# Optimization experiments

Measured on AMD Instinct MI355X. Metric: run time of the kernel, lower is better.

## Reference

```python
import jax, jax.numpy as jnp
import numpy as np

S, TM1, B, V, E, H = 96, 96, 8, 32000, 256, 512
PAD = 0
NEG = -1e30


def setup_inputs() -> dict:
    key = jax.random.key(0)
    ks = jax.random.split(key, 10)
    n = lambda k, shape, s=0.05: (jax.random.normal(k, shape, jnp.float32) * s)
    return {
        "src": jax.random.randint(ks[0], (S, B), 0, V, jnp.int32),
        "tgt": jax.random.randint(ks[1], (TM1 + 1, B), 0, V, jnp.int32),
        "emb": n(ks[2], (V, E)),
        "W_ih": n(ks[3], (4 * H, E)),
        "W_hh": n(ks[4], (4 * H, H)),
        "b_ih": jnp.zeros((4 * H,), jnp.float32),
        "b_hh": jnp.zeros((4 * H,), jnp.float32),
        "W_att": n(ks[5], (H, H)),
        "sent": n(ks[6], (H,)),
        "W_read": n(ks[7], (V, H)),
    }


def _lstm_cell(x, h, c, W_ih, W_hh, b_ih, b_hh):
    g = x @ W_ih.T + b_ih + h @ W_hh.T + b_hh
    i, f, gg, o = jnp.split(g, 4, axis=-1)
    c = jax.nn.sigmoid(f) * c + jax.nn.sigmoid(i) * jnp.tanh(gg)
    h = jax.nn.sigmoid(o) * jnp.tanh(c)
    return h, c


def _forward(src, tgt, emb, W_ih, W_hh, b_ih, b_hh, W_att, sent, W_read):
    # padding_idx behavior: pad row of embedding is zero (and gets no grad)
    emb_eff = emb * (jnp.arange(V) != PAD).astype(emb.dtype)[:, None]
    xs = jnp.concatenate([emb_eff[src], emb_eff[tgt[:-1]]], axis=0)  # [S+TM1,B,E]

    def step(carry, x):
        h, c = carry
        h, c = _lstm_cell(x, h, c, W_ih, W_hh, b_ih, b_hh)
        return (h, c), h

    init = (jnp.zeros((B, H), xs.dtype), jnp.zeros((B, H), xs.dtype))
    _, H_all = jax.lax.scan(step, init, xs)  # [S+TM1,B,H]

    H_dec = H_all[S:]                              # [TM1,B,H]
    Q = jnp.tanh(H_dec @ W_att.T)                  # [TM1,B,H]
    Z = jnp.einsum("tbh,jbh->tjb", Q, H_all)      # [TM1,S+TM1,B]
    zs = jnp.einsum("tbh,h->tb", Q, sent)         # sentinel logit
    logits = jnp.concatenate([Z, zs[:, None, :]], axis=1)  # [TM1,S+TM1+1,B]

    j = jnp.arange(S + TM1 + 1)
    t = jnp.arange(TM1)
    valid = (j[None, :] < S + t[:, None] + 1) | (j[None, :] == S + TM1)
    logits = jnp.where(valid[:, :, None], logits, NEG)
    a = jax.nn.softmax(logits, axis=1)
    a_src, a_tgt, a_sent = a[:, :S], a[:, S:S + TM1], a[:, -1]

    # pointer distributions via scatter-add (avoids dense one-hot [S,B,V])
    b_idx = jnp.arange(B)[None, None, :]
    t_idx = jnp.arange(TM1)[:, None, None]
    p_ptr = jnp.zeros((TM1, B, V), a.dtype)
    p_ptr = p_ptr.at[t_idx, b_idx, src[None, :, :]].add(a_src)
    p_ptr = p_ptr.at[t_idx, b_idx, tgt[:-1][None, :, :]].add(a_tgt)

    p_vocab = jax.nn.softmax(H_dec @ W_read.T, axis=-1)  # [TM1,B,V]
    p = p_ptr + p_vocab * a_sent[:, :, None]
    ptr_scores = p_ptr + a_sent[:, :, None]

    mask = (tgt != PAD).astype(p.dtype)  # [TM1+1,B]
    gold = jnp.take_along_axis(jnp.log(p), tgt[1:][:, :, None], axis=2)[..., 0] * mask[1:]
    gold_ptr = jnp.take_along_axis(jnp.log(ptr_scores), tgt[1:][:, :, None], axis=2)[..., 0] * mask[1:]
    return gold.sum(0), gold_ptr.sum(0)  # ([B], [B])


def reference(src, tgt, emb, W_ih, W_hh, b_ih, b_hh, W_att, sent, W_read):
    return _forward(src, tgt, emb, W_ih, W_hh, b_ih, b_hh, W_att, sent, W_read)
```

## Files before the change

### kernel.cpp

```cpp
#include <hip/hip_runtime.h>
#include <hip/hip_cooperative_groups.h>
#include <math.h>

#define SS   96
#define TM   96
#define BB   8
#define VV   32000
#define EE   256
#define HH   512
#define NTOK (SS + TM)
#define G4   (4 * HH)
#define NEGF (-1e30f)
#define NBLK 64

typedef __attribute__((ext_vector_type(8))) short short8;
typedef __attribute__((ext_vector_type(4))) float f32x4;

#define XIH_OFF   ((size_t)0)
#define XIH_SZ    ((size_t)NTOK * BB * G4)
#define HALL_OFF  (XIH_OFF + XIH_SZ)
#define HALL_SZ   ((size_t)NTOK * BB * HH)
#define Q_OFF     (HALL_OFF + HALL_SZ)
#define Q_SZ      ((size_t)TM * BB * HH)
#define PPTR_OFF  (Q_OFF + Q_SZ)
#define ASENT_OFF (PPTR_OFF + (size_t)(TM * BB))
#define SSUM_OFF  (ASENT_OFF + (size_t)(TM * BB))
#define LSTAR_OFF (SSUM_OFF + (size_t)(TM * BB))
#define BAR_OFF   (LSTAR_OFF + (size_t)(TM * BB))
#define ABF_OFF   (BAR_OFF + (size_t)1024)
#define ABF_SZF   ((size_t)(768 * HH) / 2)
#define WBF_OFF   (ABF_OFF + ABF_SZF)
#define WBF_SZF   ((size_t)VV * HH / 2)
#define NEED_F    (WBF_OFF + WBF_SZF)

__device__ __forceinline__ float sigf(float x) { return 1.f / (1.f + __expf(-x)); }

__global__ void __launch_bounds__(256) k_xih(const int* __restrict__ src,
                                             const int* __restrict__ tgt,
                                             const float* __restrict__ emb,
                                             const float* __restrict__ Wih,
                                             const float* __restrict__ bih,
                                             const float* __restrict__ bhh,
                                             float* __restrict__ xih) {
    __shared__ float xs[16][EE];
    const int tok0 = blockIdx.x * 16;
    const int row0 = blockIdx.y * 256;
    const int tid  = threadIdx.x;

    for (int e = tid; e < 16 * EE; e += 256) {
        int tk = e >> 8;
        int k  = e & 255;
        int tau = tok0 + tk;
        int idx = (tau < SS * BB) ? src[tau] : tgt[tau - SS * BB];
        xs[tk][k] = (idx == 0) ? 0.f : emb[(size_t)idx * EE + k];
    }
    __syncthreads();

    const int row = row0 + tid;
    const float bias = bih[row] + bhh[row];
    float acc[16];
#pragma unroll
    for (int r = 0; r < 16; ++r) acc[r] = bias;

    const float4* w4 = (const float4*)(Wih + (size_t)row * EE);
    for (int k4 = 0; k4 < EE / 4; ++k4) {
        float4 w = w4[k4];
#pragma unroll
        for (int r = 0; r < 16; ++r) {
            float4 x = *((const float4*)&xs[r][k4 * 4]);
            acc[r] += w.x * x.x + w.y * x.y + w.z * x.z + w.w * x.w;
        }
    }
#pragma unroll
    for (int r = 0; r < 16; ++r)
        xih[(size_t)(tok0 + r) * G4 + row] = acc[r];
}

__global__ void __launch_bounds__(256) k_lstm(const float* __restrict__ xih,
                                              const float* __restrict__ Whh,
                                              float* __restrict__ hall,
                                              unsigned* __restrict__ bar) {
    __shared__ float hb[8 * 516];

    const int tid  = threadIdx.x;
    const int gid  = blockIdx.x * 256 + tid;
    const int b    = gid & 7;
    const int gate = (gid >> 3) & 3;
    const int i    = gid >> 5;
    const int row  = gate * HH + i;
    const float4* w4 = (const float4*)(Whh + (size_t)row * HH);

    float c = 0.f;
    float xnext = xih[(size_t)(0 * BB + b) * G4 + row];

    for (int t = 0; t < NTOK; ++t) {
        float acc = xnext;
        if (t > 0) {
            const float* hprev = hall + (size_t)(t - 1) * (BB * HH);
            float tmp[16];
#pragma unroll
            for (int u = 0; u < 16; ++u)
                tmp[u] = __hip_atomic_load(hprev + tid + u * 256,
                                           __ATOMIC_RELAXED, __HIP_MEMORY_SCOPE_AGENT);
#pragma unroll
            for (int u = 0; u < 16; ++u) {
                int e = tid + u * 256;
                hb[(e >> 9) * 516 + (e & 511)] = tmp[u];
            }
            __syncthreads();

            const float4* h4 = (const float4*)(hb + b * 516);
#pragma unroll 8
            for (int k4 = 0; k4 < HH / 4; ++k4) {
                float4 w = w4[k4];
                float4 h = h4[k4];
                acc += w.x * h.x + w.y * h.y + w.z * h.z + w.w * h.w;
            }
        }
        float gf = __shfl_down(acc, 8, 64);
        float gg = __shfl_down(acc, 16, 64);
        float go = __shfl_down(acc, 24, 64);
        if (gate == 0) {
            float is = sigf(acc);
            float fs = sigf(gf);
            float gv = tanhf(gg);
            float os = sigf(go);
            c = fs * c + is * gv;
            float h = os * tanhf(c);
            __hip_atomic_store(&hall[(size_t)(t * BB + b) * HH + i], h,
                               __ATOMIC_RELAXED, __HIP_MEMORY_SCOPE_AGENT);
        }

        if (t < NTOK - 1) {
            xnext = xih[(size_t)((t + 1) * BB + b) * G4 + row];

            __syncthreads();
            const unsigned target = (unsigned)(t + 1);
            if (tid == 0)
                __hip_atomic_store(&bar[(size_t)blockIdx.x * 16], target,
                                   __ATOMIC_RELAXED, __HIP_MEMORY_SCOPE_AGENT);
            if (tid < 64) {
                while (__hip_atomic_load(&bar[(size_t)tid * 16], __ATOMIC_RELAXED,
                                         __HIP_MEMORY_SCOPE_AGENT) < target) {}
            }
            __syncthreads();
        }
    }
}

__global__ void __launch_bounds__(256) k_q(const float* __restrict__ hall,
                                           const float* __restrict__ Watt,
                                           float* __restrict__ q) {
    __shared__ float hb[8 * 516];
    const int t = blockIdx.x, tid = threadIdx.x;
    const float* hdec = hall + (size_t)(SS + t) * (BB * HH);
    for (int e = tid; e < BB * HH; e += 256)
        hb[(e >> 9) * 516 + (e & 511)] = hdec[e];
    __syncthreads();

    for (int oi = tid; oi < BB * HH; oi += 256) {
        int b = oi & 7, ii = oi >> 3;
        const float4* w4 = (const float4*)(Watt + (size_t)ii * HH);
        const float4* h4 = (const float4*)(hb + b * 516);
        float acc = 0.f;
        for (int k4 = 0; k4 < HH / 4; ++k4) {
            float4 w = w4[k4], h = h4[k4];
            acc += w.x * h.x + w.y * h.y + w.z * h.z + w.w * h.w;
        }
        q[(size_t)(t * BB + b) * HH + ii] = tanhf(acc);
    }
}

__global__ void __launch_bounds__(256) k_att(const float* __restrict__ hall,
                                             const float* __restrict__ q,
                                             const float* __restrict__ sent,
                                             const int* __restrict__ src,
                                             const int* __restrict__ tgt,
                                             float* __restrict__ pptr,
                                             float* __restrict__ asent) {
    __shared__ float qs[HH];
    __shared__ float av[256];
    __shared__ float red[256];
    const int t = blockIdx.x, b = blockIdx.y, tid = threadIdx.x;

    for (int e = tid; e < HH; e += 256) qs[e] = q[(size_t)(t * BB + b) * HH + e];
    __syncthreads();

    const int j = tid;
    float acc = NEGF;
    if (j < SS + TM + 1) {
        bool valid = (j < SS + t + 1) || (j == SS + TM);
        if (valid) {
            const float* vptr = (j < SS + TM) ? (hall + (size_t)(j * BB + b) * HH) : sent;
            const float4* v4 = (const float4*)vptr;
            const float4* q4 = (const float4*)qs;
            float a = 0.f;
            for (int k4 = 0; k4 < HH / 4; ++k4) {
                float4 v = v4[k4], qq = q4[k4];
                a += v.x * qq.x + v.y * qq.y + v.z * qq.z + v.w * qq.w;
            }
            acc = a;
        }
    }
    red[tid] = acc;
    __syncthreads();
    for (int s2 = 128; s2 > 0; s2 >>= 1) {
        if (tid < s2) red[tid] = fmaxf(red[tid], red[tid + s2]);
        __syncthreads();
    }
    float m = red[0];
    __syncthreads();
    float e = __expf(acc - m);
    red[tid] = e;
    __syncthreads();
    for (int s2 = 128; s2 > 0; s2 >>= 1) {
        if (tid < s2) red[tid] += red[tid + s2];
        __syncthreads();
    }
    float denom = red[0];
    __syncthreads();
    float a = e / denom;
    av[tid] = a;
    __syncthreads();

    const int vs = tgt[(t + 1) * BB + b];
    float contrib = 0.f;
    if (j < SS) {
        if (src[j * BB + b] == vs) contrib += av[j];
        if (tgt[j * BB + b] == vs) contrib += av[SS + j];
    }
    red[tid] = contrib;
    __syncthreads();
    for (int s2 = 128; s2 > 0; s2 >>= 1) {
        if (tid < s2) red[tid] += red[tid + s2];
        __syncthreads();
    }
    if (tid == 0) {
        pptr[t * BB + b]  = red[0];
        asent[t * BB + b] = av[SS + TM];
    }
}

__device__ __forceinline__ unsigned short f2bf(float x) {
    unsigned bits = __float_as_uint(x);
    bits += 0x7FFFu + ((bits >> 16) & 1u);
    return (unsigned short)(bits >> 16);
}
__global__ void __launch_bounds__(256) k_cvt(const float* __restrict__ Wread,
                                             const float* __restrict__ hdec,
                                             unsigned short* __restrict__ Wbf,
                                             unsigned short* __restrict__ Abf) {
    const size_t WN = (size_t)VV * HH;
    const size_t AN = (size_t)768 * HH;
    size_t base = ((size_t)blockIdx.x * 256 + threadIdx.x) * 8;
    const float* src; unsigned short* dst; size_t off;
    if (base < WN) { src = Wread; dst = Wbf; off = base; }
    else           { src = hdec;  dst = Abf; off = base - WN; if (off >= AN) return; }
    float4 f0 = *(const float4*)(src + off);
    float4 f1 = *(const float4*)(src + off + 4);
    uint4 o;
    o.x = (unsigned)f2bf(f0.x) | ((unsigned)f2bf(f0.y) << 16);
    o.y = (unsigned)f2bf(f0.z) | ((unsigned)f2bf(f0.w) << 16);
    o.z = (unsigned)f2bf(f1.x) | ((unsigned)f2bf(f1.y) << 16);
    o.w = (unsigned)f2bf(f1.z) | ((unsigned)f2bf(f1.w) << 16);
    *(uint4*)(dst + off) = o;
}

__global__ void __launch_bounds__(256) k_vocab_mfma(const unsigned short* __restrict__ Abf,
                                                    const unsigned short* __restrict__ Wbf,
                                                    const int* __restrict__ tgt,
                                                    float* __restrict__ ssum,
                                                    float* __restrict__ lstar) {
    const int tid  = threadIdx.x;
    const int wave = tid >> 6;
    const int lane = tid & 63;
    const int r16  = lane & 15;
    const int kg   = lane >> 4;
    const int n0   = blockIdx.x * 64;

    const unsigned short* b0 = Wbf + (size_t)(n0 +  0 + r16) * HH + kg * 8;
    const unsigned short* b1 = Wbf + (size_t)(n0 + 16 + r16) * HH + kg * 8;
    const unsigned short* b2 = Wbf + (size_t)(n0 + 32 + r16) * HH + kg * 8;
    const unsigned short* b3 = Wbf + (size_t)(n0 + 48 + r16) * HH + kg * 8;

    for (int pass = 0; pass < 12; ++pass) {
        const int row0 = pass * 64 + wave * 16;
        const unsigned short* arow = Abf + (size_t)(row0 + r16) * HH + kg * 8;

        f32x4 acc0 = {0.f,0.f,0.f,0.f}, acc1 = acc0, acc2 = acc0, acc3 = acc0;
#pragma unroll
        for (int ks = 0; ks < 16; ++ks) {
            short8 a = *(const short8*)(arow + ks * 32);
            acc0 = __builtin_amdgcn_mfma_f32_16x16x32_bf16(a, *(const short8*)(b0 + ks * 32), acc0, 0, 0, 0);
            acc1 = __builtin_amdgcn_mfma_f32_16x16x32_bf16(a, *(const short8*)(b1 + ks * 32), acc1, 0, 0, 0);
            acc2 = __builtin_amdgcn_mfma_f32_16x16x32_bf16(a, *(const short8*)(b2 + ks * 32), acc2, 0, 0, 0);
            acc3 = __builtin_amdgcn_mfma_f32_16x16x32_bf16(a, *(const short8*)(b3 + ks * 32), acc3, 0, 0, 0);
        }

#pragma unroll
        for (int reg = 0; reg < 4; ++reg) {
            const int rowg = row0 + 4 * kg + reg;
            const int vs = tgt[BB + rowg];
            int cg;
            cg = n0 +  0 + r16; if (cg == vs) lstar[rowg] = acc0[reg];
            cg = n0 + 16 + r16; if (cg == vs) lstar[rowg] = acc1[reg];
            cg = n0 + 32 + r16; if (cg == vs) lstar[rowg] = acc2[reg];
            cg = n0 + 48 + r16; if (cg == vs) lstar[rowg] = acc3[reg];

            float v = __expf(acc0[reg]) + __expf(acc1[reg]) +
                      __expf(acc2[reg]) + __expf(acc3[reg]);
            v += __shfl_xor(v, 1, 64);
            v += __shfl_xor(v, 2, 64);
            v += __shfl_xor(v, 4, 64);
            v += __shfl_xor(v, 8, 64);
            if (r16 == 0) atomicAdd(&ssum[rowg], v);
        }
    }
}

__global__ void __launch_bounds__(256) k_vocab_f32(const float* __restrict__ hall,
                                                   const float* __restrict__ Wread,
                                                   const int* __restrict__ tgt,
                                                   float* __restrict__ ssum,
                                                   float* __restrict__ lstar) {
    __shared__ float hs[32 * HH];
    const int tid = threadIdx.x;
    const int v0 = blockIdx.x * 512 + tid * 2;
    const int v1 = v0 + 1;
    const bool g0 = v0 < VV, g1 = v1 < VV;
    const float4* w40 = (const float4*)(Wread + (size_t)(g0 ? v0 : 0) * HH);
    const float4* w41 = (const float4*)(Wread + (size_t)(g1 ? v1 : 0) * HH);
    const int rbase0 = blockIdx.y * 128;

    for (int ch = 0; ch < 4; ++ch) {
        const int rbase = rbase0 + ch * 32;
        const float4* sp4 = (const float4*)(hall + ((size_t)SS * BB + rbase) * HH);
        float4* hs4 = (float4*)hs;
        for (int e = tid; e < 32 * HH / 4; e += 256) hs4[e] = sp4[e];
        __syncthreads();

        float acc0[32], acc1[32];
#pragma unroll
        for (int r = 0; r < 32; ++r) { acc0[r] = 0.f; acc1[r] = 0.f; }

        for (int k4 = 0; k4 < HH / 4; ++k4) {
            float4 w0 = w40[k4];
            float4 w1 = w41[k4];
#pragma unroll
            for (int r = 0; r < 32; ++r) {
                float4 h = *((const float4*)(hs + r * HH + k4 * 4));
                acc0[r] += w0.x * h.x + w0.y * h.y + w0.z * h.z + w0.w * h.w;
                acc1[r] += w1.x * h.x + w1.y * h.y + w1.z * h.z + w1.w * h.w;
            }
        }

#pragma unroll
        for (int r = 0; r < 32; ++r) {
            const int row = rbase + r;
            float val = 0.f;
            if (g0) val += __expf(acc0[r]);
            if (g1) val += __expf(acc1[r]);
#pragma unroll
            for (int d = 32; d > 0; d >>= 1) val += __shfl_xor(val, d, 64);
            if ((tid & 63) == 0) atomicAdd(&ssum[row], val);
            const int vs = tgt[row + BB];
            if (g0 && v0 == vs) lstar[row] = acc0[r];
            else if (g1 && v1 == vs) lstar[row] = acc1[r];
        }
        __syncthreads();
    }
}

__global__ void __launch_bounds__(768) k_final(const float* __restrict__ pptr,
                                               const float* __restrict__ asent,
                                               const float* __restrict__ ssum,
                                               const float* __restrict__ lstar,
                                               const int* __restrict__ tgt,
                                               float* __restrict__ out) {
    __shared__ float g[TM * BB], gp[TM * BB];
    const int tid = threadIdx.x;
    const int vs = tgt[tid + BB];
    const float pv = __expf(lstar[tid]) / ssum[tid];
    const float ps = pptr[tid];
    const float as = asent[tid];
    if (vs != 0) {
        g[tid]  = logf(ps + pv * as);
        gp[tid] = logf(ps + as);
    } else {
        g[tid] = 0.f; gp[tid] = 0.f;
    }
    __syncthreads();
    if (tid < BB) {
        float s1 = 0.f, s2 = 0.f;
        for (int t = 0; t < TM; ++t) { s1 += g[t * BB + tid]; s2 += gp[t * BB + tid]; }
        out[tid] = s1;
        out[BB + tid] = s2;
    }
}

extern "C" void kernel_launch(void* const* d_in, const int* in_sizes, int n_in,
                              void* d_out, int out_size, void* d_ws, size_t ws_size,
                              hipStream_t stream) {
    (void)in_sizes; (void)n_in; (void)out_size;
    const int*   src   = (const int*)d_in[0];
    const int*   tgt   = (const int*)d_in[1];
    const float* emb   = (const float*)d_in[2];
    const float* Wih   = (const float*)d_in[3];
    const float* Whh   = (const float*)d_in[4];
    const float* bih   = (const float*)d_in[5];
    const float* bhh   = (const float*)d_in[6];
    const float* Watt  = (const float*)d_in[7];
    const float* sent  = (const float*)d_in[8];
    const float* Wread = (const float*)d_in[9];
    float* ws  = (float*)d_ws;
    float* out = (float*)d_out;

    const bool use_mfma = ws_size >= NEED_F * sizeof(float);

    hipMemsetAsync((void*)(ws + SSUM_OFF), 0,
                   (size_t)(TM * BB * 2 + 1024) * sizeof(float), stream);

    k_xih<<<dim3(NTOK * BB / 16, G4 / 256), 256, 0, stream>>>(
        src, tgt, emb, Wih, bih, bhh, ws + XIH_OFF);

    {
        const float* xih = ws + XIH_OFF;
        const float* whh = Whh;
        float* hall = ws + HALL_OFF;
        unsigned* bar = (unsigned*)(ws + BAR_OFF);
        void* args[] = { (void*)&xih, (void*)&whh, (void*)&hall, (void*)&bar };
        hipLaunchCooperativeKernel((void*)k_lstm, dim3(NBLK), dim3(256), args, 0, stream);
    }

    if (use_mfma) {
        k_cvt<<<dim3(8192), 256, 0, stream>>>(Wread, ws + HALL_OFF + (size_t)SS * BB * HH,
                                              (unsigned short*)(ws + WBF_OFF),
                                              (unsigned short*)(ws + ABF_OFF));
    }

    k_q<<<dim3(TM), 256, 0, stream>>>(ws + HALL_OFF, Watt, ws + Q_OFF);

    k_att<<<dim3(TM, BB), 256, 0, stream>>>(ws + HALL_OFF, ws + Q_OFF, sent,
                                            src, tgt, ws + PPTR_OFF, ws + ASENT_OFF);

    if (use_mfma) {
        k_vocab_mfma<<<dim3(VV / 64), 256, 0, stream>>>(
            (const unsigned short*)(ws + ABF_OFF),
            (const unsigned short*)(ws + WBF_OFF),
            tgt, ws + SSUM_OFF, ws + LSTAR_OFF);
    } else {
        k_vocab_f32<<<dim3(63, 6), 256, 0, stream>>>(ws + HALL_OFF, Wread, tgt,
                                                     ws + SSUM_OFF, ws + LSTAR_OFF);
    }

    k_final<<<dim3(1), dim3(TM * BB), 0, stream>>>(ws + PPTR_OFF, ws + ASENT_OFF,
                                                   ws + SSUM_OFF, ws + LSTAR_OFF,
                                                   tgt, out);
}
```

Measured before the change: 1.520 ms.

## Run LSTM recurrence with register-resident bf16 W_hh and MFMA across 16 blocks

Converts W_hh to bf16 once and keeps each wave's slice of it in registers. The recurrent matvec now runs as 16x16x32 bf16 MFMAs over 16 cooperative blocks instead of 64 blocks of fp32 dot products. The hidden state is exchanged through a double-buffered, zero-padded bf16 buffer, so each step reads less data and the grid barrier spans fewer blocks. The cost is bf16 rounding inside the recurrence, which can drift over 192 steps, and a separate conversion kernel. The vocab conversion is also split into two launches.

New measurement: 1.629 ms. +7.2%, slower.

```diff
diff --git a/kernel.cpp b/kernel.cpp
--- a/kernel.cpp
+++ b/kernel.cpp
@@ -1,5 +1,4 @@
 #include <hip/hip_runtime.h>
-#include <hip/hip_cooperative_groups.h>
 #include <math.h>
 
 #define SS   96
@@ -11,10 +10,11 @@
 #define NTOK (SS + TM)
 #define G4   (4 * HH)
 #define NEGF (-1e30f)
-#define NBLK 64
+#define LBLK 16
 
 typedef __attribute__((ext_vector_type(8))) short short8;
 typedef __attribute__((ext_vector_type(4))) float f32x4;
+typedef unsigned long long u64;
 
 #define XIH_OFF   ((size_t)0)
 #define XIH_SZ    ((size_t)NTOK * BB * G4)
@@ -27,13 +27,23 @@
 #define SSUM_OFF  (ASENT_OFF + (size_t)(TM * BB))
 #define LSTAR_OFF (SSUM_OFF + (size_t)(TM * BB))
 #define BAR_OFF   (LSTAR_OFF + (size_t)(TM * BB))
-#define ABF_OFF   (BAR_OFF + (size_t)1024)
+#define WHHBF_OFF (BAR_OFF + (size_t)1024)
+#define WHHBF_SZF ((size_t)G4 * HH / 2)
+#define HBF_OFF   (WHHBF_OFF + WHHBF_SZF)
+#define HBF_SZF   ((size_t)2 * 16 * HH / 2)
+#define ABF_OFF   (HBF_OFF + HBF_SZF)
 #define ABF_SZF   ((size_t)(768 * HH) / 2)
 #define WBF_OFF   (ABF_OFF + ABF_SZF)
 #define WBF_SZF   ((size_t)VV * HH / 2)
 #define NEED_F    (WBF_OFF + WBF_SZF)
 
 __device__ __forceinline__ float sigf(float x) { return 1.f / (1.f + __expf(-x)); }
+
+__device__ __forceinline__ unsigned short f2bf(float x) {
+    unsigned bits = __float_as_uint(x);
+    bits += 0x7FFFu + ((bits >> 16) & 1u);
+    return (unsigned short)(bits >> 16);
+}
 
 __global__ void __launch_bounds__(256) k_xih(const int* __restrict__ src,
                                              const int* __restrict__ tgt,
@@ -76,73 +86,116 @@
         xih[(size_t)(tok0 + r) * G4 + row] = acc[r];
 }
 
-__global__ void __launch_bounds__(256) k_lstm(const float* __restrict__ xih,
-                                              const float* __restrict__ Whh,
-                                              float* __restrict__ hall,
-                                              unsigned* __restrict__ bar) {
-    __shared__ float hb[8 * 516];
-
-    const int tid  = threadIdx.x;
-    const int gid  = blockIdx.x * 256 + tid;
-    const int b    = gid & 7;
-    const int gate = (gid >> 3) & 3;
-    const int i    = gid >> 5;
-    const int row  = gate * HH + i;
-    const float4* w4 = (const float4*)(Whh + (size_t)row * HH);
-
-    float c = 0.f;
-    float xnext = xih[(size_t)(0 * BB + b) * G4 + row];
+__global__ void __launch_bounds__(256) k_cvt2(const float* __restrict__ src,
+                                              unsigned short* __restrict__ dst,
+                                              long n) {
+    size_t base = ((size_t)blockIdx.x * 256 + threadIdx.x) * 8;
+    if ((long)base >= n) return;
+    float4 f0 = *(const float4*)(src + base);
+    float4 f1 = *(const float4*)(src + base + 4);
+    uint4 o;
+    o.x = (unsigned)f2bf(f0.x) | ((unsigned)f2bf(f0.y) << 16);
+    o.y = (unsigned)f2bf(f0.z) | ((unsigned)f2bf(f0.w) << 16);
+    o.z = (unsigned)f2bf(f1.x) | ((unsigned)f2bf(f1.y) << 16);
+    o.w = (unsigned)f2bf(f1.z) | ((unsigned)f2bf(f1.w) << 16);
+    *(uint4*)(dst + base) = o;
+}
+
+__global__ void __launch_bounds__(256, 1) k_lstm(const float* __restrict__ xih,
+                                                 const unsigned short* __restrict__ whhbf,
+                                                 float* __restrict__ hall,
+                                                 unsigned short* __restrict__ hbf,
+                                                 unsigned* __restrict__ bar) {
+    const int tid = threadIdx.x;
+    const int wv  = tid >> 6;
+    const int l   = tid & 63;
+    const int b16 = l & 15;
+    const int kg  = l >> 4;
+    const int bb  = b16 & 7;
+    const int I0  = blockIdx.x * 32 + wv * 8;
+
+    const int j = b16;
+    const size_t ar0 = ((size_t)((j >> 3) * HH + I0 + (j & 7))) * HH + kg * 8;
+    const size_t ar1 = ((size_t)((2 + (j >> 3)) * HH + I0 + (j & 7))) * HH + kg * 8;
+    short8 A0[16], A1[16];
+#pragma unroll
+    for (int ks = 0; ks < 16; ++ks) {
+        A0[ks] = *(const short8*)(whhbf + ar0 + ks * 32);
+        A1[ks] = *(const short8*)(whhbf + ar1 + ks * 32);
+    }
+
+    if (blockIdx.x == 0) {
+        u64* pad0 = (u64*)(hbf + 8 * HH);
+        u64* pad1 = (u64*)(hbf + 16 * HH + 8 * HH);
+        for (int e = tid; e < (8 * HH) / 4; e += 256) {
+            __hip_atomic_store(pad0 + e, 0ULL, __ATOMIC_RELAXED, __HIP_MEMORY_SCOPE_AGENT);
+            __hip_atomic_store(pad1 + e, 0ULL, __ATOMIC_RELAXED, __HIP_MEMORY_SCOPE_AGENT);
+        }
+    }
+
+    const int xgate0 = (kg >> 1);
+    const int xgate1 = 2 + (kg >> 1);
+    const int xi     = I0 + (kg & 1) * 4;
+
+    float c0[4] = {0.f, 0.f, 0.f, 0.f};
 
     for (int t = 0; t < NTOK; ++t) {
-        float acc = xnext;
+        const float* xbase = xih + ((size_t)t * BB + bb) * G4;
+        float4 x0 = *(const float4*)(xbase + xgate0 * HH + xi);
+        float4 x1 = *(const float4*)(xbase + xgate1 * HH + xi);
+        f32x4 acc0 = {x0.x, x0.y, x0.z, x0.w};
+        f32x4 acc1 = {x1.x, x1.y, x1.z, x1.w};
+
         if (t > 0) {
-            const float* hprev = hall + (size_t)(t - 1) * (BB * HH);
-            float tmp[16];
-#pragma unroll
-            for (int u = 0; u < 16; ++u)
-                tmp[u] = __hip_atomic_load(hprev + tid + u * 256,
-                                           __ATOMIC_RELAXED, __HIP_MEMORY_SCOPE_AGENT);
-#pragma unroll
-            for (int u = 0; u < 16; ++u) {
-                int e = tid + u * 256;
-                hb[(e >> 9) * 516 + (e & 511)] = tmp[u];
+            const unsigned short* hsrc = hbf + ((t - 1) & 1) * (16 * HH) + b16 * HH + kg * 8;
+            u64 blo[16], bhi[16];
+#pragma unroll
+            for (int ks = 0; ks < 16; ++ks) {
+                const u64* bp = (const u64*)(hsrc + ks * 32);
+                blo[ks] = __hip_atomic_load(bp,     __ATOMIC_RELAXED, __HIP_MEMORY_SCOPE_AGENT);
+                bhi[ks] = __hip_atomic_load(bp + 1, __ATOMIC_RELAXED, __HIP_MEMORY_SCOPE_AGENT);
             }
+#pragma unroll
+            for (int ks = 0; ks < 16; ++ks) {
+                union alignas(16) { u64 q[2]; short8 s; } u;
+                u.q[0] = blo[ks]; u.q[1] = bhi[ks];
+                acc0 = __builtin_amdgcn_mfma_f32_16x16x32_bf16(A0[ks], u.s, acc0, 0, 0, 0);
+                acc1 = __builtin_amdgcn_mfma_f32_16x16x32_bf16(A1[ks], u.s, acc1, 0, 0, 0);
+            }
+        }
+
+        float hreg[4];
+#pragma unroll
+        for (int r = 0; r < 4; ++r) {
+            float gf = __shfl_down(acc0[r], 32, 64);
+            float go = __shfl_down(acc1[r], 32, 64);
+            float is = sigf(acc0[r]);
+            float fs = sigf(gf);
+            float gv = tanhf(acc1[r]);
+            float os = sigf(go);
+            c0[r] = fs * c0[r] + is * gv;
+            hreg[r] = os * tanhf(c0[r]);
+        }
+
+        if (l < 32 && b16 < BB) {
+            const int ib = I0 + kg * 4;
+            *(float4*)(hall + ((size_t)t * BB + b16) * HH + ib) =
+                make_float4(hreg[0], hreg[1], hreg[2], hreg[3]);
+            u64 pk = (u64)f2bf(hreg[0]) | ((u64)f2bf(hreg[1]) << 16) |
+                     ((u64)f2bf(hreg[2]) << 32) | ((u64)f2bf(hreg[3]) << 48);
+            __hip_atomic_store((u64*)(hbf + (t & 1) * (16 * HH) + b16 * HH + ib), pk,
+                               __ATOMIC_RELAXED, __HIP_MEMORY_SCOPE_AGENT);
+        }
+
+        if (t < NTOK - 1) {
             __syncthreads();
-
-            const float4* h4 = (const float4*)(hb + b * 516);
-#pragma unroll 8
-            for (int k4 = 0; k4 < HH / 4; ++k4) {
-                float4 w = w4[k4];
-                float4 h = h4[k4];
-                acc += w.x * h.x + w.y * h.y + w.z * h.z + w.w * h.w;
-            }
-        }
-        float gf = __shfl_down(acc, 8, 64);
-        float gg = __shfl_down(acc, 16, 64);
-        float go = __shfl_down(acc, 24, 64);
-        if (gate == 0) {
-            float is = sigf(acc);
-            float fs = sigf(gf);
-            float gv = tanhf(gg);
-            float os = sigf(go);
-            c = fs * c + is * gv;
-            float h = os * tanhf(c);
-            __hip_atomic_store(&hall[(size_t)(t * BB + b) * HH + i], h,
-                               __ATOMIC_RELAXED, __HIP_MEMORY_SCOPE_AGENT);
-        }
-
-        if (t < NTOK - 1) {
-            xnext = xih[(size_t)((t + 1) * BB + b) * G4 + row];
-
-            __syncthreads();
-            const unsigned target = (unsigned)(t + 1);
+            const unsigned tgt = (unsigned)(t + 1);
             if (tid == 0)
-                __hip_atomic_store(&bar[(size_t)blockIdx.x * 16], target,
+                __hip_atomic_store(&bar[(size_t)blockIdx.x * 16], tgt,
                                    __ATOMIC_RELAXED, __HIP_MEMORY_SCOPE_AGENT);
-            if (tid < 64) {
+            if (tid < LBLK)
                 while (__hip_atomic_load(&bar[(size_t)tid * 16], __ATOMIC_RELAXED,
-                                         __HIP_MEMORY_SCOPE_AGENT) < target) {}
-            }
+                                         __HIP_MEMORY_SCOPE_AGENT) < tgt) {}
             __syncthreads();
         }
     }
@@ -239,31 +292,6 @@
         pptr[t * BB + b]  = red[0];
         asent[t * BB + b] = av[SS + TM];
     }
-}
-
-__device__ __forceinline__ unsigned short f2bf(float x) {
-    unsigned bits = __float_as_uint(x);
-    bits += 0x7FFFu + ((bits >> 16) & 1u);
-    return (unsigned short)(bits >> 16);
-}
-__global__ void __launch_bounds__(256) k_cvt(const float* __restrict__ Wread,
-                                             const float* __restrict__ hdec,
-                                             unsigned short* __restrict__ Wbf,
-                                             unsigned short* __restrict__ Abf) {
-    const size_t WN = (size_t)VV * HH;
-    const size_t AN = (size_t)768 * HH;
-    size_t base = ((size_t)blockIdx.x * 256 + threadIdx.x) * 8;
-    const float* src; unsigned short* dst; size_t off;
-    if (base < WN) { src = Wread; dst = Wbf; off = base; }
-    else           { src = hdec;  dst = Abf; off = base - WN; if (off >= AN) return; }
-    float4 f0 = *(const float4*)(src + off);
-    float4 f1 = *(const float4*)(src + off + 4);
-    uint4 o;
-    o.x = (unsigned)f2bf(f0.x) | ((unsigned)f2bf(f0.y) << 16);
-    o.y = (unsigned)f2bf(f0.z) | ((unsigned)f2bf(f0.w) << 16);
-    o.z = (unsigned)f2bf(f1.x) | ((unsigned)f2bf(f1.y) << 16);
-    o.w = (unsigned)f2bf(f1.z) | ((unsigned)f2bf(f1.w) << 16);
-    *(uint4*)(dst + off) = o;
 }
 
 __global__ void __launch_bounds__(256) k_vocab_mfma(const unsigned short* __restrict__ Abf,
@@ -415,7 +443,7 @@
     float* ws  = (float*)d_ws;
     float* out = (float*)d_out;
 
-    const bool use_mfma = ws_size >= NEED_F * sizeof(float);
+    const bool use_mfma_vocab = ws_size >= NEED_F * sizeof(float);
 
     hipMemsetAsync((void*)(ws + SSUM_OFF), 0,
                    (size_t)(TM * BB * 2 + 1024) * sizeof(float), stream);
@@ -423,19 +451,17 @@
     k_xih<<<dim3(NTOK * BB / 16, G4 / 256), 256, 0, stream>>>(
         src, tgt, emb, Wih, bih, bhh, ws + XIH_OFF);
 
+    k_cvt2<<<dim3((unsigned)((size_t)G4 * HH / 8 / 256)), 256, 0, stream>>>(
+        Whh, (unsigned short*)(ws + WHHBF_OFF), (long)G4 * HH);
+
     {
         const float* xih = ws + XIH_OFF;
-        const float* whh = Whh;
+        const unsigned short* whhbf = (const unsigned short*)(ws + WHHBF_OFF);
         float* hall = ws + HALL_OFF;
+        unsigned short* hbf = (unsigned short*)(ws + HBF_OFF);
         unsigned* bar = (unsigned*)(ws + BAR_OFF);
-        void* args[] = { (void*)&xih, (void*)&whh, (void*)&hall, (void*)&bar };
-        hipLaunchCooperativeKernel((void*)k_lstm, dim3(NBLK), dim3(256), args, 0, stream);
-    }
-
-    if (use_mfma) {
-        k_cvt<<<dim3(8192), 256, 0, stream>>>(Wread, ws + HALL_OFF + (size_t)SS * BB * HH,
-                                              (unsigned short*)(ws + WBF_OFF),
-                                              (unsigned short*)(ws + ABF_OFF));
+        void* args[] = { (void*)&xih, (void*)&whhbf, (void*)&hall, (void*)&hbf, (void*)&bar };
+        hipLaunchCooperativeKernel((void*)k_lstm, dim3(LBLK), dim3(256), args, 0, stream);
     }
 
     k_q<<<dim3(TM), 256, 0, stream>>>(ws + HALL_OFF, Watt, ws + Q_OFF);
@@ -443,7 +469,12 @@
     k_att<<<dim3(TM, BB), 256, 0, stream>>>(ws + HALL_OFF, ws + Q_OFF, sent,
                                             src, tgt, ws + PPTR_OFF, ws + ASENT_OFF);
 
-    if (use_mfma) {
+    if (use_mfma_vocab) {
+        k_cvt2<<<dim3((unsigned)((size_t)VV * HH / 8 / 256)), 256, 0, stream>>>(
+            Wread, (unsigned short*)(ws + WBF_OFF), (long)VV * HH);
+        k_cvt2<<<dim3((unsigned)((size_t)768 * HH / 8 / 256)), 256, 0, stream>>>(
+            ws + HALL_OFF + (size_t)SS * BB * HH, (unsigned short*)(ws + ABF_OFF),
+            (long)768 * HH);
         k_vocab_mfma<<<dim3(VV / 64), 256, 0, stream>>>(
             (const unsigned short*)(ws + ABF_OFF),
             (const unsigned short*)(ws + WBF_OFF),
```
